# Kernel tuning notes

Hardware: AMD Instinct MI355X
Metric: run time of the kernel (lower is better)

The kernel has to match this reference:

```python
import jax, jax.numpy as jnp
import numpy as np
from jax import lax

B, T, L = 16, 200, 250
IDIM, ODIM, DUNITS = 512, 80, 1024
ATT_DIM, ACONV_CHANS, ACONV_K = 128, 32, 31
PRENET = 256


def setup_inputs() -> dict:
    key = jax.random.key(0)
    ks = iter(jax.random.split(key, 40))
    def nrm(shape, fan_in):
        return jax.random.normal(next(ks), shape, jnp.float32) * (fan_in ** -0.5)
    inp = {}
    inp['hs'] = jax.random.normal(next(ks), (B, T, IDIM), jnp.float32)
    inp['hlens'] = jax.random.randint(next(ks), (B,), T // 2, T + 1)
    inp['ys'] = jax.random.normal(next(ks), (B, L, ODIM), jnp.float32)
    # location-aware attention params
    inp['W_enc'] = nrm((IDIM, ATT_DIM), IDIM)
    inp['b_enc'] = jnp.zeros((ATT_DIM,), jnp.float32)
    inp['W_dec'] = nrm((DUNITS, ATT_DIM), DUNITS)
    inp['W_att'] = nrm((ACONV_CHANS, ATT_DIM), ACONV_CHANS)
    inp['loc_conv_w'] = nrm((ACONV_CHANS, 1, ACONV_K), ACONV_K)
    inp['gvec_w'] = nrm((ATT_DIM,), ATT_DIM)
    inp['gvec_b'] = jnp.zeros((), jnp.float32)
    # prenet (no bias, dropout off in eval)
    inp['prenet_W1'] = nrm((ODIM, PRENET), ODIM)
    inp['prenet_W2'] = nrm((PRENET, PRENET), PRENET)
    # LSTM cells (torch gate order i,f,g,o; bih+bhh folded into one bias)
    in0 = IDIM + PRENET
    inp['Wih0'] = nrm((4 * DUNITS, in0), in0)
    inp['Whh0'] = nrm((4 * DUNITS, DUNITS), DUNITS)
    inp['b0'] = jnp.zeros((4 * DUNITS,), jnp.float32)
    inp['Wih1'] = nrm((4 * DUNITS, DUNITS), DUNITS)
    inp['Whh1'] = nrm((4 * DUNITS, DUNITS), DUNITS)
    inp['b1'] = jnp.zeros((4 * DUNITS,), jnp.float32)
    # output heads
    inp['feat_W'] = nrm((DUNITS, ODIM), DUNITS)
    inp['prob_W'] = nrm((DUNITS,), DUNITS)
    inp['prob_b'] = jnp.zeros((), jnp.float32)
    # postnet: conv(no bias) + BN(eval; running mean=0, var=1 folded away) + tanh
    inp['post_w_in'] = nrm((512, ODIM, 5), 5 * ODIM)
    inp['post_g_in'] = jnp.ones((512,), jnp.float32)
    inp['post_b_in'] = jnp.zeros((512,), jnp.float32)
    inp['post_w_mid'] = nrm((3, 512, 512, 5), 5 * 512)
    inp['post_g_mid'] = jnp.ones((3, 512), jnp.float32)
    inp['post_b_mid'] = jnp.zeros((3, 512), jnp.float32)
    inp['post_w_out'] = nrm((ODIM, 512, 5), 5 * 512)
    inp['post_g_out'] = jnp.ones((ODIM,), jnp.float32)
    inp['post_b_out'] = jnp.zeros((ODIM,), jnp.float32)
    return inp


def _conv1d(x, w, pad):
    # x: [B, Cin, T], w: [Cout, Cin, K]
    return lax.conv_general_dilated(x, w, (1,), [(pad, pad)],
                                    dimension_numbers=('NCH', 'OIH', 'NCH'))


def _lstm(x, h, c, Wih, Whh, b):
    g = x @ Wih.T + h @ Whh.T + b
    i, f, gg, o = jnp.split(g, 4, axis=-1)
    c2 = jax.nn.sigmoid(f) * c + jax.nn.sigmoid(i) * jnp.tanh(gg)
    return jax.nn.sigmoid(o) * jnp.tanh(c2), c2


def reference(hs, hlens, ys, W_enc, b_enc, W_dec, W_att, loc_conv_w, gvec_w, gvec_b,
              prenet_W1, prenet_W2, Wih0, Whh0, b0, Wih1, Whh1, b1,
              feat_W, prob_W, prob_b,
              post_w_in, post_g_in, post_b_in, post_w_mid, post_g_mid, post_b_mid,
              post_w_out, post_g_out, post_b_out):
    mask = jnp.arange(T)[None, :] < hlens[:, None]            # [B,T]
    pre_enc = hs @ W_enc + b_enc                              # [B,T,A] precomputed
    # teacher forcing: prenet input at step i is ys[:, i-1] (zeros at i=0);
    # prenet has no recurrent dependency -> vectorize over time
    prev = jnp.concatenate([jnp.zeros((B, 1, ODIM), hs.dtype), ys[:, :L - 1]], axis=1)
    pren = jax.nn.relu(jax.nn.relu(prev @ prenet_W1) @ prenet_W2)  # [B,L,256]
    att_w0 = mask.astype(hs.dtype) / hlens[:, None].astype(hs.dtype)
    z = jnp.zeros((B, DUNITS), hs.dtype)
    carry0 = (z, z, z, z, att_w0)

    def step(carry, pren_t):
        z0, c0, z1, c1, att_w = carry
        conv = _conv1d(att_w[:, None, :], loc_conv_w, ACONV_K // 2)   # [B,C,T]
        e = jnp.tanh(pre_enc + jnp.einsum('bct,ca->bta', conv, W_att)
                     + (z0 @ W_dec)[:, None, :]) @ gvec_w + gvec_b    # [B,T]
        e = jnp.where(mask, e, -1e30)
        w = jax.nn.softmax(2.0 * e, axis=1)                           # scaling=2.0
        att_c = jnp.einsum('bt,btd->bd', w, hs)
        x = jnp.concatenate([att_c, pren_t], axis=1)
        z0n, c0n = _lstm(x, z0, c0, Wih0, Whh0, b0)
        z1n, c1n = _lstm(z0n, z1, c1, Wih1, Whh1, b1)
        return (z0n, c0n, z1n, c1n, w), (z1n @ feat_W, z1n @ prob_W + prob_b)

    _, (outs, probs) = lax.scan(step, carry0, jnp.swapaxes(pren, 0, 1))
    outs = jnp.transpose(outs, (1, 2, 0))   # [B, odim, L] (matches torch.stack dim=2)
    probs = probs.T                         # [B, L]
    # postnet (BN in eval with running mean=0/var=1 reduces to gamma*x+beta)
    h = jnp.tanh(post_g_in[:, None] * _conv1d(outs, post_w_in, 2) + post_b_in[:, None])
    for i in range(3):
        h = jnp.tanh(post_g_mid[i][:, None] * _conv1d(h, post_w_mid[i], 2)
                     + post_b_mid[i][:, None])
    h = post_g_out[:, None] * _conv1d(h, post_w_out, 2) + post_b_out[:, None]
    post_outs = outs + h
    return jnp.swapaxes(post_outs, 1, 2), jnp.swapaxes(outs, 1, 2), probs
```

## Files before the change

kernel.cpp:

```cpp
#include <hip/hip_runtime.h>
#include <cstdint>
#include <cstddef>

constexpr int B_ = 16, T_ = 200, L_ = 250;
constexpr int IDIM = 512, ODIM = 80, DUNITS = 1024;
constexpr int ADIM = 128, ACH = 32, AK = 31;
constexpr int PRE = 256;
constexpr int TPAD = 208;

typedef _Float16 h16;
typedef _Float16 half8 __attribute__((ext_vector_type(8)));
typedef _Float16 half4 __attribute__((ext_vector_type(4)));
typedef float f32x4 __attribute__((ext_vector_type(4)));

constexpr int FSTEP = 800;
constexpr int FZ0W = 0, FDPW = 256, FAW = 288;

constexpr size_t OFF_PE    = 0;
constexpr size_t OFF_H0H   = 851968;
constexpr size_t OFF_Z1H   = 917504;
constexpr size_t OFF_ATTC  = 983040;
constexpr size_t OFF_DP    = 999424;
constexpr size_t OFF_FLAGS = 1007616;
constexpr size_t ZERO_BYTES= 1807616;
constexpr size_t OFF_MB    = 1807616;
constexpr size_t OFF_WDR   = 1815808;
constexpr size_t OFF_PREN  = 2077952;
constexpr size_t OFF_HSH   = 4125952;
constexpr size_t OFF_W0AH  = 7402752;
constexpr size_t OFF_WHH0  = 13694208;
constexpr size_t OFF_WI1   = 22082816;
constexpr size_t OFF_WHH1  = 30471424;
constexpr size_t OFF_Z1ALL = 38860032;
constexpr size_t OFF_OUTS  = 47052032;
constexpr size_t OFF_PA    = 48332032;
constexpr size_t OFF_PB    = 56524032;

__device__ __forceinline__ float fsig(float x) {
  x = fminf(fmaxf(x, -30.f), 30.f);
  return __builtin_amdgcn_rcpf(1.f + __expf(-x));
}
__device__ __forceinline__ float ftanh(float x) {
  x = fminf(fmaxf(x, -15.f), 15.f);
  const float e = __expf(2.f * x);
  return (e - 1.f) * __builtin_amdgcn_rcpf(e + 1.f);
}
__device__ __forceinline__ f32x4 mfma16(half8 a, half8 b, f32x4 c) {
  return __builtin_amdgcn_mfma_f32_16x16x32_f16(a, b, c, 0, 0, 0);
}
__device__ __forceinline__ half8 load8_agent(const h16* p) {
  union { unsigned long long q[2]; half8 v; } cv;
  cv.q[0] = __hip_atomic_load((const unsigned long long*)p, __ATOMIC_RELAXED,
                              __HIP_MEMORY_SCOPE_AGENT);
  cv.q[1] = __hip_atomic_load(((const unsigned long long*)p) + 1, __ATOMIC_RELAXED,
                              __HIP_MEMORY_SCOPE_AGENT);
  return cv.v;
}
__device__ __forceinline__ float loadf_agent(const float* p) {
  union { unsigned u; float f; } cv;
  cv.u = __hip_atomic_load((const unsigned*)p, __ATOMIC_RELAXED,
                           __HIP_MEMORY_SCOPE_AGENT);
  return cv.f;
}
__device__ __forceinline__ void storef_agent(float* p, float v) {
  union { unsigned u; float f; } cv; cv.f = v;
  __hip_atomic_store((unsigned*)p, cv.u, __ATOMIC_RELAXED, __HIP_MEMORY_SCOPE_AGENT);
}
__device__ __forceinline__ int loadw(const int* p) {
  return __hip_atomic_load(p, __ATOMIC_RELAXED, __HIP_MEMORY_SCOPE_AGENT);
}
__device__ __forceinline__ void storew(int* p, int v) {
  __hip_atomic_store(p, v, __ATOMIC_RELAXED, __HIP_MEMORY_SCOPE_AGENT);
}
__device__ __forceinline__ void poll_n(const int* base, const int n) {
  if ((int)threadIdx.x < n) {
    const int* f = base + threadIdx.x;
    while (loadw(f) == 0) __builtin_amdgcn_s_sleep(1);
  }
  __syncthreads();
  __builtin_amdgcn_sched_barrier(0);
}
__device__ __forceinline__ void poll_all256(const int* base) {
  const int* f = base + threadIdx.x;
  while (loadw(f) == 0) __builtin_amdgcn_s_sleep(1);
  __syncthreads();
  __builtin_amdgcn_sched_barrier(0);
}


__global__ void k_zero(float4* __restrict__ p, int n4) {
  const int i = blockIdx.x * blockDim.x + threadIdx.x;
  if (i < n4) p[i] = make_float4(0.f, 0.f, 0.f, 0.f);
}

__global__ void __launch_bounds__(128) k_preenc(const float* __restrict__ hs,
    const float* __restrict__ W_enc, const float* __restrict__ b_enc,
    h16* __restrict__ pe_h) {
  const int bt = blockIdx.x, b = bt / T_, tt = bt % T_;
  __shared__ float s[IDIM];
  for (int i = threadIdx.x; i < IDIM; i += 128) s[i] = hs[(size_t)bt * IDIM + i];
  __syncthreads();
  const int a = threadIdx.x;
  float acc = b_enc[a];
#pragma unroll 4
  for (int d = 0; d < IDIM; ++d) acc += s[d] * W_enc[d * ADIM + a];
  pe_h[((size_t)b * ADIM + a) * TPAD + tt] = (h16)acc;
}

__global__ void k_precMb(const float* __restrict__ lconv, const float* __restrict__ W_att,
                         h16* __restrict__ Mb) {
  const int at = blockIdx.x, lane = threadIdx.x;
  const int a = at * 16 + (lane & 15);
  const int k0 = (lane >> 4) * 8;
  half8 o;
#pragma unroll
  for (int j = 0; j < 8; ++j) {
    const int k = k0 + j;
    float v = 0.f;
    if (k < AK)
      for (int c = 0; c < ACH; ++c) v += lconv[c * AK + k] * W_att[c * ADIM + a];
    o[j] = (h16)v;
  }
  *(half8*)(Mb + (size_t)(at * 64 + lane) * 8) = o;
}

__global__ void k_cvt_perm(const float* __restrict__ src, h16* __restrict__ dst,
                           const int K) {
  const int rr = blockIdx.x;
  const int u = rr >> 2, g = rr & 3;
  const float* s = src + (size_t)(g * 1024 + u) * K;
  h16* d = dst + (size_t)rr * K;
  for (int k = threadIdx.x; k < K; k += 256) d[k] = (h16)s[k];
}

__global__ void k_cvt_wdec(const float* __restrict__ Wdec, h16* __restrict__ Wdr) {
  const int a = blockIdx.x;
  for (int k = threadIdx.x; k < 1024; k += 256)
    Wdr[(size_t)a * 1024 + k] = (h16)Wdec[(size_t)k * ADIM + a];
}

__global__ void k_cvt_f32f16(const float* __restrict__ src, h16* __restrict__ dst) {
  const size_t i = ((size_t)blockIdx.x * 256 + threadIdx.x) * 4;
  const float4 v = *(const float4*)(src + i);
  half4 o; o[0] = (h16)v.x; o[1] = (h16)v.y; o[2] = (h16)v.z; o[3] = (h16)v.w;
  *(half4*)(dst + i) = o;
}

__global__ void k_prenet1(const float* __restrict__ ys, const float* __restrict__ W1,
                          float* __restrict__ h1) {
  const int bl = blockIdx.x, b = bl / L_, l = bl % L_;
  __shared__ float s[ODIM];
  if (threadIdx.x < ODIM)
    s[threadIdx.x] = (l == 0) ? 0.f : ys[((size_t)b * L_ + l - 1) * ODIM + threadIdx.x];
  __syncthreads();
  const int p = threadIdx.x;
  float acc = 0.f;
#pragma unroll 4
  for (int o = 0; o < ODIM; ++o) acc += s[o] * W1[o * PRE + p];
  h1[(size_t)bl * PRE + p] = fmaxf(acc, 0.f);
}

__global__ void k_prenet2h(const float* __restrict__ h1, const float* __restrict__ W2,
                           h16* __restrict__ pren_h) {
  const int bl = blockIdx.x, b = bl / L_, ll = bl % L_;
  __shared__ float s[PRE];
  s[threadIdx.x] = h1[(size_t)bl * PRE + threadIdx.x];
  __syncthreads();
  const int p = threadIdx.x;
  float acc = 0.f;
#pragma unroll 4
  for (int o = 0; o < PRE; ++o) acc += s[o] * W2[o * PRE + p];
  pren_h[((size_t)ll * B_ + b) * PRE + p] = (h16)fmaxf(acc, 0.f);
}


struct ScanP {
  const h16 *pe_h, *Mb, *Wdr, *hs_h, *pren_h;
  const h16 *W0ah, *Whh0h, *Wz01h, *Whh1h;
  h16 *h0h, *z1h, *attc;
  float *dp;
  const float *gvw, *b0, *b1;
  const int *hlens;
  h16 *z1all;
  int *flags;
};

__device__ __forceinline__ void lstm0_partA(const h16* pren_t, const h16* z0p,
    const half8 wA[6], const half8 wH[8], f32x4& acc) {
  const int lane = threadIdx.x & 63, wave = threadIdx.x >> 6;
  const int nloc = lane & 15, kl8 = (lane >> 4) * 8;
  half8 rz[8];
#pragma unroll
  for (int c = 0; c < 8; ++c)
    rz[c] = load8_agent(z0p + nloc * DUNITS + wave * 256 + c * 32 + kl8);
#pragma unroll
  for (int c = 0; c < 8; ++c) acc = mfma16(rz[c], wH[c], acc);
#pragma unroll
  for (int c = 0; c < 6; ++c) {
    const int kg = wave * 192 + c * 32;
    if (kg >= 512)
      acc = mfma16(*(const half8*)(pren_t + nloc * PRE + (kg - 512) + kl8), wA[c], acc);
  }
}

__device__ __forceinline__ void lstm0_partB(const ScanP& P,
    h16* z0o, const int slab, const half8 wA[6], float& c0reg, f32x4 acc,
    float sred[4][64][5], float sg[16][20], h16* sho) {
  const int tid = threadIdx.x;
  const int lane = tid & 63, wave = tid >> 6;
  const int nloc = lane & 15, kl8 = (lane >> 4) * 8;
  half8 ra[6];
#pragma unroll
  for (int c = 0; c < 6; ++c) {
    const int kg = wave * 192 + c * 32;
    if (kg < 512) ra[c] = load8_agent(P.attc + nloc * IDIM + kg + kl8);
  }
#pragma unroll
  for (int c = 0; c < 6; ++c) {
    const int kg = wave * 192 + c * 32;
    if (kg < 512) acc = mfma16(ra[c], wA[c], acc);
  }
#pragma unroll
  for (int r = 0; r < 4; ++r) sred[wave][lane][r] = acc[r];
  __syncthreads();
  {
    const float v = sred[0][lane][wave] + sred[1][lane][wave]
                  + sred[2][lane][wave] + sred[3][lane][wave];
    sg[lane & 15][4 * (lane >> 4) + wave] = v;
  }
  __syncthreads();
  if (tid < 64) {
    const int ul = tid >> 4, b = tid & 15;
    const int u = slab * 4 + ul;
    const float xi = sg[ul * 4 + 0][b] + P.b0[u];
    const float xf = sg[ul * 4 + 1][b] + P.b0[1024 + u];
    const float xg = sg[ul * 4 + 2][b] + P.b0[2048 + u];
    const float xo = sg[ul * 4 + 3][b] + P.b0[3072 + u];
    const float cn = fsig(xf) * c0reg + fsig(xi) * ftanh(xg);
    c0reg = cn;
    sho[ul * 16 + b] = (h16)(fsig(xo) * ftanh(cn));
  }
  __syncthreads();
  if (tid < 16) {
    union { h16 h[4]; unsigned long long q; } u4;
#pragma unroll
    for (int j = 0; j < 4; ++j) u4.h[j] = sho[j * 16 + tid];
    __hip_atomic_store((unsigned long long*)(z0o + tid * DUNITS + slab * 4), u4.q,
                       __ATOMIC_RELAXED, __HIP_MEMORY_SCOPE_AGENT);
  }
}

__device__ __forceinline__ void lstm1_mm(const ScanP& P, const half8 r0[8],
    const half8 r1[8], h16* z1o, h16* z1all_s, const int slab,
    const half8 wI[8], const half8 wHH[8], float& c1reg,
    float sred[4][64][5], float sg[16][20], h16* sho) {
  const int tid = threadIdx.x;
  const int lane = tid & 63, wave = tid >> 6;
  f32x4 acc = {0.f, 0.f, 0.f, 0.f};
#pragma unroll
  for (int c = 0; c < 8; ++c) acc = mfma16(r0[c], wI[c], acc);
#pragma unroll
  for (int c = 0; c < 8; ++c) acc = mfma16(r1[c], wHH[c], acc);
#pragma unroll
  for (int r = 0; r < 4; ++r) sred[wave][lane][r] = acc[r];
  __syncthreads();
  {
    const float v = sred[0][lane][wave] + sred[1][lane][wave]
                  + sred[2][lane][wave] + sred[3][lane][wave];
    sg[lane & 15][4 * (lane >> 4) + wave] = v;
  }
  __syncthreads();
  if (tid < 64) {
    const int ul = tid >> 4, b = tid & 15;
    const int u = slab * 4 + ul;
    const float xi = sg[ul * 4 + 0][b] + P.b1[u];
    const float xf = sg[ul * 4 + 1][b] + P.b1[1024 + u];
    const float xg = sg[ul * 4 + 2][b] + P.b1[2048 + u];
    const float xo = sg[ul * 4 + 3][b] + P.b1[3072 + u];
    const float cn = fsig(xf) * c1reg + fsig(xi) * ftanh(xg);
    c1reg = cn;
    const float hn = fsig(xo) * ftanh(cn);
    const h16 hh = (h16)hn;
    z1all_s[b * DUNITS + u] = hh;
    sho[ul * 16 + b] = hh;
  }
  __syncthreads();
  if (tid < 16) {
    union { h16 h[4]; unsigned long long q; } u4;
#pragma unroll
    for (int j = 0; j < 4; ++j) u4.h[j] = sho[j * 16 + tid];
    __hip_atomic_store((unsigned long long*)(z1o + tid * DUNITS + slab * 4), u4.q,
                       __ATOMIC_RELAXED, __HIP_MEMORY_SCOPE_AGENT);
  }
}

__global__ void __launch_bounds__(256, 1) k_scan(const ScanP P) {
  __shared__ float s_red[4][64][5];
  __shared__ float s_g[16][20];
  __shared__ h16   s_ho[64];
  __shared__ float s_aw[240];
  __shared__ float s_dp[ADIM];
  __shared__ float s_gv[ADIM];
  __shared__ float s_ew[256];
  __shared__ float s_wt[208];
  __shared__ float s_par[4][512];
  __shared__ float s_r8[8];
  __shared__ float s_bc[2];
  __shared__ float s_cvpe[13][8][64][4];

  const int blk = blockIdx.x, tid = threadIdx.x;
  const int lane = tid & 63, wave = tid >> 6;
  constexpr int BD = B_ * DUNITS;

  if (blk < 16) {
    const int b = blk;
    const int hl = P.hlens[b];
    const int mtmax = (hl + 15) >> 4;
    const int slab = 240 + b;
    const int l15 = lane & 15;
    half8 bfrag[8];
#pragma unroll
    for (int at = 0; at < 8; ++at)
      bfrag[at] = *(const half8*)(P.Mb + (size_t)(at * 64 + lane) * 8);
    half8 wA[6], wH[8];
    {
      const int nloc = lane & 15, kl8 = (lane >> 4) * 8;
      const h16* wrA = P.W0ah + ((size_t)(slab * 16 + nloc)) * 768 + wave * 192 + kl8;
      const h16* wrH = P.Whh0h + ((size_t)(slab * 16 + nloc)) * 1024 + wave * 256 + kl8;
#pragma unroll
      for (int c = 0; c < 6; ++c) wA[c] = *(const half8*)(wrA + c * 32);
#pragma unroll
      for (int c = 0; c < 8; ++c) wH[c] = *(const half8*)(wrH + c * 32);
    }
    if (tid < 240) {
      const int tt = tid - 15;
      s_aw[tid] = (tt >= 0 && tt < hl) ? (1.f / (float)hl) : 0.f;
    }
    if (tid < ADIM) s_gv[tid] = P.gvw[tid];
    __syncthreads();
    float c0reg = 0.f;

    for (int mi = 0; mi < 4; ++mi) {
      const int mt = wave + mi * 4;
      if (mt < mtmax) {
        half8 af;
#pragma unroll
        for (int j = 0; j < 8; ++j)
          af[j] = (h16)s_aw[mt * 16 + l15 + (lane >> 4) * 8 + j];
        const int t0 = mt * 16 + 4 * (lane >> 4);
        half4 pe[8];
#pragma unroll
        for (int at = 0; at < 8; ++at)
          pe[at] = *(const half4*)(P.pe_h + ((size_t)b * ADIM + at * 16 + l15) * TPAD + t0);
#pragma unroll
        for (int at = 0; at < 8; ++at) {
          f32x4 z4 = {0.f, 0.f, 0.f, 0.f};
          const f32x4 cv = mfma16(af, bfrag[at], z4);
          float4 o;
          o.x = cv[0] + (float)pe[at][0]; o.y = cv[1] + (float)pe[at][1];
          o.z = cv[2] + (float)pe[at][2]; o.w = cv[3] + (float)pe[at][3];
          *(float4*)&s_cvpe[mt][at][lane][0] = o;
        }
      }
    }
    __syncthreads();

    for (int i = 0; i < L_; ++i) {
      const h16* z0p = P.h0h + (size_t)(i & 1) * BD;
      h16* z0o = P.h0h + (size_t)((i & 1) ^ 1) * BD;
      int* sf = P.flags + (size_t)i * FSTEP;
      poll_n(sf + FDPW, 8);
      if (tid < ADIM) s_dp[tid] = loadf_agent(P.dp + b * ADIM + tid);
      __syncthreads();
#pragma unroll
      for (int mi = 0; mi < 4; ++mi) {
        const int mt = wave + mi * 4;
        if (mt < mtmax) {
          const int t0 = mt * 16 + 4 * (lane >> 4);
          float e0 = 0.f, e1 = 0.f, e2 = 0.f, e3 = 0.f;
#pragma unroll
          for (int at = 0; at < 8; ++at) {
            const float4 v = *(const float4*)&s_cvpe[mt][at][lane][0];
            const int a = at * 16 + l15;
            const float g = s_gv[a], d = s_dp[a];
            e0 += g * ftanh(v.x + d);
            e1 += g * ftanh(v.y + d);
            e2 += g * ftanh(v.z + d);
            e3 += g * ftanh(v.w + d);
          }
#pragma unroll
          for (int o = 1; o < 16; o <<= 1) {
            e0 += __shfl_xor(e0, o); e1 += __shfl_xor(e1, o);
            e2 += __shfl_xor(e2, o); e3 += __shfl_xor(e3, o);
          }
          if (l15 == 0) {
            s_ew[t0 + 0] = e0; s_ew[t0 + 1] = e1; s_ew[t0 + 2] = e2; s_ew[t0 + 3] = e3;
          }
        }
      }
      __syncthreads();
      const float val = (tid < hl) ? 2.f * s_ew[tid] : -3.0e38f;
      float m = val;
#pragma unroll
      for (int o = 32; o > 0; o >>= 1) m = fmaxf(m, __shfl_xor(m, o));
      if ((tid & 63) == 0) s_r8[tid >> 6] = m;
      __syncthreads();
      if (tid == 0) s_bc[0] = fmaxf(fmaxf(s_r8[0], s_r8[1]), fmaxf(s_r8[2], s_r8[3]));
      __syncthreads();
      const float pp = (tid < hl) ? __expf(val - s_bc[0]) : 0.f;
      float ssum = pp;
#pragma unroll
      for (int o = 32; o > 0; o >>= 1) ssum += __shfl_xor(ssum, o);
      if ((tid & 63) == 0) s_r8[4 + (tid >> 6)] = ssum;
      __syncthreads();
      if (tid == 0) s_bc[1] = __builtin_amdgcn_rcpf(s_r8[4] + s_r8[5] + s_r8[6] + s_r8[7]);
      __syncthreads();
      if (tid < T_) {
        const float w = pp * s_bc[1];
        s_wt[tid] = w;
        s_aw[15 + tid] = w;
      }
      __syncthreads();
      const h16* hsb = P.hs_h + (size_t)b * T_ * IDIM;
      {
        const int d0 = lane * 8;
        const h16* hp = hsb + d0;
        float a8[8] = {0.f, 0.f, 0.f, 0.f, 0.f, 0.f, 0.f, 0.f};
        int tt = wave;
        for (; tt + 12 < hl; tt += 16) {
          const half8 h0 = *(const half8*)(hp + (size_t)tt * IDIM);
          const half8 h1 = *(const half8*)(hp + (size_t)(tt + 4) * IDIM);
          const half8 h2 = *(const half8*)(hp + (size_t)(tt + 8) * IDIM);
          const half8 h3 = *(const half8*)(hp + (size_t)(tt + 12) * IDIM);
          const float w0 = s_wt[tt], w1 = s_wt[tt + 4];
          const float w2 = s_wt[tt + 8], w3 = s_wt[tt + 12];
#pragma unroll
          for (int j = 0; j < 8; ++j)
            a8[j] += w0 * (float)h0[j] + w1 * (float)h1[j]
                   + w2 * (float)h2[j] + w3 * (float)h3[j];
        }
        for (; tt < hl; tt += 4) {
          const half8 hv = *(const half8*)(hp + (size_t)tt * IDIM);
          const float wt = s_wt[tt];
#pragma unroll
          for (int j = 0; j < 8; ++j) a8[j] += wt * (float)hv[j];
        }
#pragma unroll
        for (int j = 0; j < 8; ++j) s_par[wave][d0 + j] = a8[j];
      }
      __syncthreads();
      {
        const int d = tid * 2;
        const float cx0 = s_par[0][d] + s_par[1][d] + s_par[2][d] + s_par[3][d];
        const float cx1 = s_par[0][d + 1] + s_par[1][d + 1] + s_par[2][d + 1]
                        + s_par[3][d + 1];
        union { h16 h[2]; unsigned u; } cv;
        cv.h[0] = (h16)cx0; cv.h[1] = (h16)cx1;
        __hip_atomic_store((unsigned*)(P.attc + b * IDIM + d), cv.u,
                           __ATOMIC_RELAXED, __HIP_MEMORY_SCOPE_AGENT);
      }
      asm volatile("s_waitcnt vmcnt(0)" ::: "memory");
      __syncthreads();
      if (tid < 16) storew(sf + FAW + tid * 32 + b, 1);
      f32x4 acc0 = {0.f, 0.f, 0.f, 0.f};
      lstm0_partA(P.pren_h + (size_t)i * (B_ * PRE), z0p, wA, wH, acc0);
      poll_n(sf + FAW + (blk & 15) * 32, 16);
      lstm0_partB(P, z0o, slab, wA, c0reg, acc0, s_red, s_g, s_ho);
      asm volatile("s_waitcnt vmcnt(0)" ::: "memory");
      __syncthreads();
      if (tid == 0) storew(sf + FZ0W + blk, 1);
      for (int mi = 0; mi < 4; ++mi) {
        const int mt = wave + mi * 4;
        if (mt < mtmax) {
          half8 af;
#pragma unroll
          for (int j = 0; j < 8; ++j)
            af[j] = (h16)s_aw[mt * 16 + l15 + (lane >> 4) * 8 + j];
          const int t0 = mt * 16 + 4 * (lane >> 4);
          half4 pe[8];
#pragma unroll
          for (int at = 0; at < 8; ++at)
            pe[at] = *(const half4*)(P.pe_h + ((size_t)b * ADIM + at * 16 + l15) * TPAD + t0);
#pragma unroll
          for (int at = 0; at < 8; ++at) {
            f32x4 z4 = {0.f, 0.f, 0.f, 0.f};
            const f32x4 cv = mfma16(af, bfrag[at], z4);
            float4 o;
            o.x = cv[0] + (float)pe[at][0]; o.y = cv[1] + (float)pe[at][1];
            o.z = cv[2] + (float)pe[at][2]; o.w = cv[3] + (float)pe[at][3];
            *(float4*)&s_cvpe[mt][at][lane][0] = o;
          }
        }
      }
      __syncthreads();
    }
    return;
  }

  const int g = blk - 16;
  const bool dbl = (g < 16);
  const bool isdp = (g >= 16 && g < 24);
  half8 wA0[6], wH0[8], wI1a[8], wHH1a[8], wI1b[8], wHH1b[8], wD[8];
  {
    const int nloc = lane & 15, kl8 = (lane >> 4) * 8;
    const h16* wrA = P.W0ah + ((size_t)(g * 16 + nloc)) * 768 + wave * 192 + kl8;
    const h16* wrH = P.Whh0h + ((size_t)(g * 16 + nloc)) * 1024 + wave * 256 + kl8;
    const h16* wrI = P.Wz01h + ((size_t)(g * 16 + nloc)) * 1024 + wave * 256 + kl8;
    const h16* wrX = P.Whh1h + ((size_t)(g * 16 + nloc)) * 1024 + wave * 256 + kl8;
#pragma unroll
    for (int c = 0; c < 6; ++c) wA0[c] = *(const half8*)(wrA + c * 32);
#pragma unroll
    for (int c = 0; c < 8; ++c) wH0[c] = *(const half8*)(wrH + c * 32);
#pragma unroll
    for (int c = 0; c < 8; ++c) wI1a[c] = *(const half8*)(wrI + c * 32);
#pragma unroll
    for (int c = 0; c < 8; ++c) wHH1a[c] = *(const half8*)(wrX + c * 32);
    if (dbl) {
      const h16* wrI2 = P.Wz01h + ((size_t)((240 + g) * 16 + nloc)) * 1024 + wave * 256 + kl8;
      const h16* wrX2 = P.Whh1h + ((size_t)((240 + g) * 16 + nloc)) * 1024 + wave * 256 + kl8;
#pragma unroll
      for (int c = 0; c < 8; ++c) wI1b[c] = *(const half8*)(wrI2 + c * 32);
#pragma unroll
      for (int c = 0; c < 8; ++c) wHH1b[c] = *(const half8*)(wrX2 + c * 32);
    }
    if (isdp) {
      const h16* wrD = P.Wdr + ((size_t)((g - 16) * 16 + nloc)) * 1024 + wave * 256 + kl8;
#pragma unroll
      for (int c = 0; c < 8; ++c) wD[c] = *(const half8*)(wrD + c * 32);
    }
  }
  float c0reg = 0.f, c1a = 0.f, c1b = 0.f;
  const int nloc = lane & 15, kl8 = (lane >> 4) * 8;

  for (int i = 0; i < L_; ++i) {
    const h16* z0p = P.h0h + (size_t)(i & 1) * BD;
    h16* z0o = P.h0h + (size_t)((i & 1) ^ 1) * BD;
    const h16* z1p = P.z1h + (size_t)((i & 1) ^ 1) * BD;
    h16* z1o = P.z1h + (size_t)(i & 1) * BD;
    int* sf = P.flags + (size_t)i * FSTEP;
    if (i > 0) poll_all256(P.flags + (size_t)(i - 1) * FSTEP + FZ0W);
    if (isdp) {
      half8 rz[8];
#pragma unroll
      for (int c = 0; c < 8; ++c)
        rz[c] = load8_agent(z0p + nloc * DUNITS + wave * 256 + c * 32 + kl8);
      f32x4 acc = {0.f, 0.f, 0.f, 0.f};
#pragma unroll
      for (int c = 0; c < 8; ++c) acc = mfma16(rz[c], wD[c], acc);
#pragma unroll
      for (int r = 0; r < 4; ++r) s_red[wave][lane][r] = acc[r];
      __syncthreads();
      {
        const float v = s_red[0][lane][wave] + s_red[1][lane][wave]
                      + s_red[2][lane][wave] + s_red[3][lane][wave];
        const int row = lane & 15, batch = 4 * (lane >> 4) + wave;
        storef_agent(P.dp + batch * ADIM + (g - 16) * 16 + row, v);
      }
      asm volatile("s_waitcnt vmcnt(0)" ::: "memory");
      __syncthreads();
      if (tid == 0) storew(sf + FDPW + (g - 16), 1);
    }
    if (i > 0) {
      half8 r0[8], r1[8];
#pragma unroll
      for (int c = 0; c < 8; ++c)
        r0[c] = load8_agent(z0p + nloc * DUNITS + wave * 256 + c * 32 + kl8);
#pragma unroll
      for (int c = 0; c < 8; ++c)
        r1[c] = load8_agent(z1p + nloc * DUNITS + wave * 256 + c * 32 + kl8);
      h16* z1s = P.z1all + (size_t)(i - 1) * BD;
      lstm1_mm(P, r0, r1, z1o, z1s, g, wI1a, wHH1a, c1a, s_red, s_g, s_ho);
      if (dbl)
        lstm1_mm(P, r0, r1, z1o, z1s, 240 + g, wI1b, wHH1b, c1b, s_red, s_g, s_ho);
    }
    f32x4 acc0 = {0.f, 0.f, 0.f, 0.f};
    lstm0_partA(P.pren_h + (size_t)i * (B_ * PRE), z0p, wA0, wH0, acc0);
    poll_n(sf + FAW + (blk & 15) * 32, 16);
    lstm0_partB(P, z0o, g, wA0, c0reg, acc0, s_red, s_g, s_ho);
    asm volatile("s_waitcnt vmcnt(0)" ::: "memory");
    __syncthreads();
    if (tid == 0) storew(sf + FZ0W + blk, 1);
  }
  poll_all256(P.flags + (size_t)(L_ - 1) * FSTEP + FZ0W);
  {
    const h16* z0p = P.h0h + (size_t)(L_ & 1) * BD;
    const h16* z1p = P.z1h + (size_t)((L_ & 1) ^ 1) * BD;
    h16* z1o = P.z1h + (size_t)(L_ & 1) * BD;
    h16* z1s = P.z1all + (size_t)(L_ - 1) * BD;
    half8 r0[8], r1[8];
#pragma unroll
    for (int c = 0; c < 8; ++c)
      r0[c] = load8_agent(z0p + nloc * DUNITS + wave * 256 + c * 32 + kl8);
#pragma unroll
    for (int c = 0; c < 8; ++c)
      r1[c] = load8_agent(z1p + nloc * DUNITS + wave * 256 + c * 32 + kl8);
    lstm1_mm(P, r0, r1, z1o, z1s, g, wI1a, wHH1a, c1a, s_red, s_g, s_ho);
    if (dbl)
      lstm1_mm(P, r0, r1, z1o, z1s, 240 + g, wI1b, wHH1b, c1b, s_red, s_g, s_ho);
  }
}


__global__ void __launch_bounds__(128) k_heads(const h16* __restrict__ z1_all,
    const float* __restrict__ feat_W, const float* __restrict__ prob_W,
    const float* __restrict__ prob_b, float* __restrict__ out1,
    float* __restrict__ probs, float* __restrict__ outs_bct) {
  const int bl = blockIdx.x, b = bl / L_, l = bl % L_;
  __shared__ float s_z[DUNITS];
  const h16* z = z1_all + ((size_t)l * B_ + b) * DUNITS;
  for (int i = threadIdx.x; i < DUNITS; i += 128) s_z[i] = (float)z[i];
  __syncthreads();
  const int co = threadIdx.x;
  if (co < ODIM) {
    float acc = 0.f;
#pragma unroll 4
    for (int d = 0; d < DUNITS; ++d) acc += s_z[d] * feat_W[d * ODIM + co];
    out1[((size_t)b * L_ + l) * ODIM + co] = acc;
    outs_bct[((size_t)b * ODIM + co) * L_ + l] = acc;
  } else if (co == 96) {
    float acc = prob_b[0];
#pragma unroll 4
    for (int d = 0; d < DUNITS; ++d) acc += s_z[d] * prob_W[d];
    probs[(size_t)b * L_ + l] = acc;
  }
}

template <bool TANH, bool FINAL>
__global__ void __launch_bounds__(256) k_conv(const float* __restrict__ x,
    const float* __restrict__ w, const float* __restrict__ gamma,
    const float* __restrict__ beta, float* __restrict__ y,
    const float* __restrict__ res, float* __restrict__ out0,
    const int Cin, const int Cout) {
  const int b = blockIdx.x;
  const int co0 = blockIdx.y * 8;
  const int tid = threadIdx.x;
  const int l = tid & 127;
  const int cg = tid >> 7;
  __shared__ float s_x[8][260];
  __shared__ float s_w[8][8][5];
  float acc[4][2] = {{0.f, 0.f}, {0.f, 0.f}, {0.f, 0.f}, {0.f, 0.f}};
  for (int ci0 = 0; ci0 < Cin; ci0 += 8) {
    __syncthreads();
    for (int i = tid; i < 8 * 260; i += 256) {
      const int ci = i / 260, col = i % 260;
      const int ll = col - 2;
      s_x[ci][col] = (ll >= 0 && ll < L_) ? x[((size_t)b * Cin + ci0 + ci) * L_ + ll] : 0.f;
    }
    for (int i = tid; i < 8 * 8 * 5; i += 256) {
      const int ci = i / 40, rem = i % 40, cl = rem / 5, k = rem % 5;
      s_w[ci][cl][k] = w[((size_t)(co0 + cl) * Cin + ci0 + ci) * 5 + k];
    }
    __syncthreads();
#pragma unroll 2
    for (int ci = 0; ci < 8; ++ci) {
      float xv0[5], xv1[5];
#pragma unroll
      for (int k = 0; k < 5; ++k) { xv0[k] = s_x[ci][l + k]; xv1[k] = s_x[ci][l + 128 + k]; }
#pragma unroll
      for (int j = 0; j < 4; ++j) {
        const int cl = cg * 4 + j;
#pragma unroll
        for (int k = 0; k < 5; ++k) {
          const float ww = s_w[ci][cl][k];
          acc[j][0] += ww * xv0[k];
          acc[j][1] += ww * xv1[k];
        }
      }
    }
  }
#pragma unroll
  for (int j = 0; j < 4; ++j) {
    const int co = co0 + cg * 4 + j;
    const float gm = gamma[co], bt = beta[co];
#pragma unroll
    for (int h = 0; h < 2; ++h) {
      const int ll = l + h * 128;
      if (ll < L_) {
        float v = gm * acc[j][h] + bt;
        if (TANH) v = ftanh(v);
        if (FINAL) out0[((size_t)b * L_ + ll) * ODIM + co] =
                       res[((size_t)b * ODIM + co) * L_ + ll] + v;
        else y[((size_t)b * Cout + co) * L_ + ll] = v;
      }
    }
  }
}


extern "C" void kernel_launch(void* const* d_in, const int* in_sizes, int n_in,
                              void* d_out, int out_size, void* d_ws, size_t ws_size,
                              hipStream_t stream) {
  const float* hs    = (const float*)d_in[0];
  const int*   hlens = (const int*)d_in[1];
  const float* ys    = (const float*)d_in[2];
  const float* W_enc = (const float*)d_in[3];
  const float* b_enc = (const float*)d_in[4];
  const float* W_dec = (const float*)d_in[5];
  const float* W_att = (const float*)d_in[6];
  const float* lconv = (const float*)d_in[7];
  const float* gvw   = (const float*)d_in[8];
  const float* pW1   = (const float*)d_in[10];
  const float* pW2   = (const float*)d_in[11];
  const float* Wih0  = (const float*)d_in[12];
  const float* Whh0  = (const float*)d_in[13];
  const float* b0    = (const float*)d_in[14];
  const float* Wih1  = (const float*)d_in[15];
  const float* Whh1  = (const float*)d_in[16];
  const float* b1    = (const float*)d_in[17];
  const float* featW = (const float*)d_in[18];
  const float* probW = (const float*)d_in[19];
  const float* probB = (const float*)d_in[20];
  const float* pwin  = (const float*)d_in[21];
  const float* pgin  = (const float*)d_in[22];
  const float* pbin  = (const float*)d_in[23];
  const float* pwmid = (const float*)d_in[24];
  const float* pgmid = (const float*)d_in[25];
  const float* pbmid = (const float*)d_in[26];
  const float* pwout = (const float*)d_in[27];
  const float* pgout = (const float*)d_in[28];
  const float* pbout = (const float*)d_in[29];

  char* ws = (char*)d_ws;
  h16*   pe_h   = (h16*)(ws + OFF_PE);
  h16*   h0h    = (h16*)(ws + OFF_H0H);
  h16*   z1h    = (h16*)(ws + OFF_Z1H);
  h16*   attc_h = (h16*)(ws + OFF_ATTC);
  float* dp     = (float*)(ws + OFF_DP);
  int*   flags  = (int*)(ws + OFF_FLAGS);
  h16*   Mb     = (h16*)(ws + OFF_MB);
  h16*   Wdr    = (h16*)(ws + OFF_WDR);
  h16*   pren_h = (h16*)(ws + OFF_PREN);
  h16*   hs_h   = (h16*)(ws + OFF_HSH);
  h16*   W0ah   = (h16*)(ws + OFF_W0AH);
  h16*   Whh0h  = (h16*)(ws + OFF_WHH0);
  h16*   Wz01h  = (h16*)(ws + OFF_WI1);
  h16*   Whh1h  = (h16*)(ws + OFF_WHH1);
  h16*   z1all  = (h16*)(ws + OFF_Z1ALL);
  float* outsb  = (float*)(ws + OFF_OUTS);
  float* pa     = (float*)(ws + OFF_PA);
  float* pb     = (float*)(ws + OFF_PB);

  float* out0 = (float*)d_out;
  float* out1 = out0 + (size_t)B_ * L_ * ODIM;
  float* out2 = out1 + (size_t)B_ * L_ * ODIM;

  hipLaunchKernelGGL(k_zero, dim3((ZERO_BYTES / 16 + 255) / 256), dim3(256), 0, stream,
                     (float4*)ws, (int)(ZERO_BYTES / 16));
  hipLaunchKernelGGL(k_preenc, dim3(B_ * T_), dim3(128), 0, stream, hs, W_enc, b_enc, pe_h);
  hipLaunchKernelGGL(k_precMb, dim3(8), dim3(64), 0, stream, lconv, W_att, Mb);
  hipLaunchKernelGGL(k_cvt_perm, dim3(4096), dim3(256), 0, stream, Wih0, W0ah, 768);
  hipLaunchKernelGGL(k_cvt_perm, dim3(4096), dim3(256), 0, stream, Whh0, Whh0h, 1024);
  hipLaunchKernelGGL(k_cvt_perm, dim3(4096), dim3(256), 0, stream, Wih1, Wz01h, 1024);
  hipLaunchKernelGGL(k_cvt_perm, dim3(4096), dim3(256), 0, stream, Whh1, Whh1h, 1024);
  hipLaunchKernelGGL(k_cvt_wdec, dim3(128), dim3(256), 0, stream, W_dec, Wdr);
  hipLaunchKernelGGL(k_cvt_f32f16, dim3(1600), dim3(256), 0, stream, hs, hs_h);
  hipLaunchKernelGGL(k_prenet1, dim3(B_ * L_), dim3(PRE), 0, stream, ys, pW1, pa);
  hipLaunchKernelGGL(k_prenet2h, dim3(B_ * L_), dim3(PRE), 0, stream, pa, pW2, pren_h);

  ScanP S{pe_h, Mb, Wdr, hs_h, pren_h, W0ah, Whh0h, Wz01h, Whh1h,
          h0h, z1h, attc_h, dp, gvw, b0, b1, hlens, z1all, flags};
  hipLaunchKernelGGL(k_scan, dim3(256), dim3(256), 0, stream, S);

  hipLaunchKernelGGL(k_heads, dim3(B_ * L_), dim3(128), 0, stream,
                     z1all, featW, probW, probB, out1, out2, outsb);

  hipLaunchKernelGGL((k_conv<true, false>), dim3(B_, 64), dim3(256), 0, stream,
                     outsb, pwin, pgin, pbin, pa, nullptr, nullptr, ODIM, 512);
  hipLaunchKernelGGL((k_conv<true, false>), dim3(B_, 64), dim3(256), 0, stream,
                     pa, pwmid, pgmid, pbmid, pb, nullptr, nullptr, 512, 512);
  hipLaunchKernelGGL((k_conv<true, false>), dim3(B_, 64), dim3(256), 0, stream,
                     pb, pwmid + (size_t)512 * 512 * 5, pgmid + 512, pbmid + 512,
                     pa, nullptr, nullptr, 512, 512);
  hipLaunchKernelGGL((k_conv<true, false>), dim3(B_, 64), dim3(256), 0, stream,
                     pa, pwmid + (size_t)2 * 512 * 512 * 5, pgmid + 1024, pbmid + 1024,
                     pb, nullptr, nullptr, 512, 512);
  hipLaunchKernelGGL((k_conv<false, true>), dim3(B_, 10), dim3(256), 0, stream,
                     pb, pwout, pgout, pbout, nullptr, outsb, out0, 512, ODIM);
}
```

Baseline: 6.994 ms.

## Compute decoder attention projection locally in attention blocks instead of via dp blocks

Result: slower. 7.307 ms (+4.5%).

```diff
diff --git a/kernel.cpp b/kernel.cpp
--- a/kernel.cpp
+++ b/kernel.cpp
@@ -13,28 +13,27 @@
 typedef _Float16 half4 __attribute__((ext_vector_type(4)));
 typedef float f32x4 __attribute__((ext_vector_type(4)));
 
-constexpr int FSTEP = 800;
-constexpr int FZ0W = 0, FDPW = 256, FAW = 288;
+constexpr int FSTEP = 768;
+constexpr int FZ0W = 0, FAW = 256;
 
 constexpr size_t OFF_PE    = 0;
 constexpr size_t OFF_H0H   = 851968;
 constexpr size_t OFF_Z1H   = 917504;
 constexpr size_t OFF_ATTC  = 983040;
-constexpr size_t OFF_DP    = 999424;
-constexpr size_t OFF_FLAGS = 1007616;
-constexpr size_t ZERO_BYTES= 1807616;
-constexpr size_t OFF_MB    = 1807616;
-constexpr size_t OFF_WDR   = 1815808;
-constexpr size_t OFF_PREN  = 2077952;
-constexpr size_t OFF_HSH   = 4125952;
-constexpr size_t OFF_W0AH  = 7402752;
-constexpr size_t OFF_WHH0  = 13694208;
-constexpr size_t OFF_WI1   = 22082816;
-constexpr size_t OFF_WHH1  = 30471424;
-constexpr size_t OFF_Z1ALL = 38860032;
-constexpr size_t OFF_OUTS  = 47052032;
-constexpr size_t OFF_PA    = 48332032;
-constexpr size_t OFF_PB    = 56524032;
+constexpr size_t OFF_FLAGS = 999424;
+constexpr size_t ZERO_BYTES= 1767424;
+constexpr size_t OFF_MB    = 1767424;
+constexpr size_t OFF_WDH   = 1775616;
+constexpr size_t OFF_PREN  = 2037760;
+constexpr size_t OFF_HSH   = 4085760;
+constexpr size_t OFF_W0AH  = 7362560;
+constexpr size_t OFF_WHH0  = 13654016;
+constexpr size_t OFF_WI1   = 22042624;
+constexpr size_t OFF_WHH1  = 30431232;
+constexpr size_t OFF_Z1ALL = 38819840;
+constexpr size_t OFF_OUTS  = 47011840;
+constexpr size_t OFF_PA    = 48291840;
+constexpr size_t OFF_PB    = 56483840;
 
 __device__ __forceinline__ float fsig(float x) {
   x = fminf(fmaxf(x, -30.f), 30.f);
@@ -56,16 +55,6 @@
                               __HIP_MEMORY_SCOPE_AGENT);
   return cv.v;
 }
-__device__ __forceinline__ float loadf_agent(const float* p) {
-  union { unsigned u; float f; } cv;
-  cv.u = __hip_atomic_load((const unsigned*)p, __ATOMIC_RELAXED,
-                           __HIP_MEMORY_SCOPE_AGENT);
-  return cv.f;
-}
-__device__ __forceinline__ void storef_agent(float* p, float v) {
-  union { unsigned u; float f; } cv; cv.f = v;
-  __hip_atomic_store((unsigned*)p, cv.u, __ATOMIC_RELAXED, __HIP_MEMORY_SCOPE_AGENT);
-}
 __device__ __forceinline__ int loadw(const int* p) {
   return __hip_atomic_load(p, __ATOMIC_RELAXED, __HIP_MEMORY_SCOPE_AGENT);
 }
@@ -133,12 +122,6 @@
   for (int k = threadIdx.x; k < K; k += 256) d[k] = (h16)s[k];
 }
 
-__global__ void k_cvt_wdec(const float* __restrict__ Wdec, h16* __restrict__ Wdr) {
-  const int a = blockIdx.x;
-  for (int k = threadIdx.x; k < 1024; k += 256)
-    Wdr[(size_t)a * 1024 + k] = (h16)Wdec[(size_t)k * ADIM + a];
-}
-
 __global__ void k_cvt_f32f16(const float* __restrict__ src, h16* __restrict__ dst) {
   const size_t i = ((size_t)blockIdx.x * 256 + threadIdx.x) * 4;
   const float4 v = *(const float4*)(src + i);
@@ -175,10 +158,9 @@
 
 
 struct ScanP {
-  const h16 *pe_h, *Mb, *Wdr, *hs_h, *pren_h;
+  const h16 *pe_h, *Mb, *Wdh, *hs_h, *pren_h;
   const h16 *W0ah, *Whh0h, *Wz01h, *Whh1h;
   h16 *h0h, *z1h, *attc;
-  float *dp;
   const float *gvw, *b0, *b1;
   const int *hlens;
   h16 *z1all;
@@ -304,6 +286,7 @@
   __shared__ float s_ew[256];
   __shared__ float s_wt[208];
   __shared__ float s_par[4][512];
+  __shared__ h16   s_z0h[DUNITS];
   __shared__ float s_r8[8];
   __shared__ float s_bc[2];
   __shared__ float s_cvpe[13][8][64][4];
@@ -369,8 +352,39 @@
       const h16* z0p = P.h0h + (size_t)(i & 1) * BD;
       h16* z0o = P.h0h + (size_t)((i & 1) ^ 1) * BD;
       int* sf = P.flags + (size_t)i * FSTEP;
-      poll_n(sf + FDPW, 8);
-      if (tid < ADIM) s_dp[tid] = loadf_agent(P.dp + b * ADIM + tid);
+      if (i > 0) poll_all256(P.flags + (size_t)(i - 1) * FSTEP + FZ0W);
+      if (tid < 128)
+        *(half8*)(s_z0h + tid * 8) = load8_agent(z0p + b * DUNITS + tid * 8);
+      __syncthreads();
+      {
+        const int kq = tid >> 4, ao = (tid & 15) * 8;
+        const h16* wp = P.Wdh + (size_t)(kq * 64) * ADIM + ao;
+        float a8[8] = {0.f, 0.f, 0.f, 0.f, 0.f, 0.f, 0.f, 0.f};
+#pragma unroll
+        for (int k0 = 0; k0 < 64; k0 += 8) {
+          half8 wv[8];
+#pragma unroll
+          for (int j = 0; j < 8; ++j)
+            wv[j] = *(const half8*)(wp + (size_t)(k0 + j) * ADIM);
+#pragma unroll
+          for (int j = 0; j < 8; ++j) {
+            const float z = (float)s_z0h[kq * 64 + k0 + j];
+#pragma unroll
+            for (int q = 0; q < 8; ++q) a8[q] += z * (float)wv[j][q];
+          }
+        }
+        float* s16 = &s_par[0][0];
+#pragma unroll
+        for (int q = 0; q < 8; ++q) s16[kq * 128 + ao + q] = a8[q];
+      }
+      __syncthreads();
+      if (tid < ADIM) {
+        const float* s16 = &s_par[0][0];
+        float s = 0.f;
+#pragma unroll
+        for (int q = 0; q < 16; ++q) s += s16[q * 128 + tid];
+        s_dp[tid] = s;
+      }
       __syncthreads();
 #pragma unroll
       for (int mi = 0; mi < 4; ++mi) {
@@ -499,8 +513,7 @@
 
   const int g = blk - 16;
   const bool dbl = (g < 16);
-  const bool isdp = (g >= 16 && g < 24);
-  half8 wA0[6], wH0[8], wI1a[8], wHH1a[8], wI1b[8], wHH1b[8], wD[8];
+  half8 wA0[6], wH0[8], wI1a[8], wHH1a[8], wI1b[8], wHH1b[8];
   {
     const int nloc = lane & 15, kl8 = (lane >> 4) * 8;
     const h16* wrA = P.W0ah + ((size_t)(g * 16 + nloc)) * 768 + wave * 192 + kl8;
@@ -522,11 +535,6 @@
       for (int c = 0; c < 8; ++c) wI1b[c] = *(const half8*)(wrI2 + c * 32);
 #pragma unroll
       for (int c = 0; c < 8; ++c) wHH1b[c] = *(const half8*)(wrX2 + c * 32);
-    }
-    if (isdp) {
-      const h16* wrD = P.Wdr + ((size_t)((g - 16) * 16 + nloc)) * 1024 + wave * 256 + kl8;
-#pragma unroll
-      for (int c = 0; c < 8; ++c) wD[c] = *(const half8*)(wrD + c * 32);
     }
   }
   float c0reg = 0.f, c1a = 0.f, c1b = 0.f;
@@ -539,27 +547,6 @@
     h16* z1o = P.z1h + (size_t)(i & 1) * BD;
     int* sf = P.flags + (size_t)i * FSTEP;
     if (i > 0) poll_all256(P.flags + (size_t)(i - 1) * FSTEP + FZ0W);
-    if (isdp) {
-      half8 rz[8];
-#pragma unroll
-      for (int c = 0; c < 8; ++c)
-        rz[c] = load8_agent(z0p + nloc * DUNITS + wave * 256 + c * 32 + kl8);
-      f32x4 acc = {0.f, 0.f, 0.f, 0.f};
-#pragma unroll
-      for (int c = 0; c < 8; ++c) acc = mfma16(rz[c], wD[c], acc);
-#pragma unroll
-      for (int r = 0; r < 4; ++r) s_red[wave][lane][r] = acc[r];
-      __syncthreads();
-      {
-        const float v = s_red[0][lane][wave] + s_red[1][lane][wave]
-                      + s_red[2][lane][wave] + s_red[3][lane][wave];
-        const int row = lane & 15, batch = 4 * (lane >> 4) + wave;
-        storef_agent(P.dp + batch * ADIM + (g - 16) * 16 + row, v);
-      }
-      asm volatile("s_waitcnt vmcnt(0)" ::: "memory");
-      __syncthreads();
-      if (tid == 0) storew(sf + FDPW + (g - 16), 1);
-    }
     if (i > 0) {
       half8 r0[8], r1[8];
 #pragma unroll
@@ -725,10 +712,9 @@
   h16*   h0h    = (h16*)(ws + OFF_H0H);
   h16*   z1h    = (h16*)(ws + OFF_Z1H);
   h16*   attc_h = (h16*)(ws + OFF_ATTC);
-  float* dp     = (float*)(ws + OFF_DP);
   int*   flags  = (int*)(ws + OFF_FLAGS);
   h16*   Mb     = (h16*)(ws + OFF_MB);
-  h16*   Wdr    = (h16*)(ws + OFF_WDR);
+  h16*   Wdh    = (h16*)(ws + OFF_WDH);
   h16*   pren_h = (h16*)(ws + OFF_PREN);
   h16*   hs_h   = (h16*)(ws + OFF_HSH);
   h16*   W0ah   = (h16*)(ws + OFF_W0AH);
@@ -752,13 +738,13 @@
   hipLaunchKernelGGL(k_cvt_perm, dim3(4096), dim3(256), 0, stream, Whh0, Whh0h, 1024);
   hipLaunchKernelGGL(k_cvt_perm, dim3(4096), dim3(256), 0, stream, Wih1, Wz01h, 1024);
   hipLaunchKernelGGL(k_cvt_perm, dim3(4096), dim3(256), 0, stream, Whh1, Whh1h, 1024);
-  hipLaunchKernelGGL(k_cvt_wdec, dim3(128), dim3(256), 0, stream, W_dec, Wdr);
+  hipLaunchKernelGGL(k_cvt_f32f16, dim3(128), dim3(256), 0, stream, W_dec, Wdh);
   hipLaunchKernelGGL(k_cvt_f32f16, dim3(1600), dim3(256), 0, stream, hs, hs_h);
   hipLaunchKernelGGL(k_prenet1, dim3(B_ * L_), dim3(PRE), 0, stream, ys, pW1, pa);
   hipLaunchKernelGGL(k_prenet2h, dim3(B_ * L_), dim3(PRE), 0, stream, pa, pW2, pren_h);
 
-  ScanP S{pe_h, Mb, Wdr, hs_h, pren_h, W0ah, Whh0h, Wz01h, Whh1h,
-          h0h, z1h, attc_h, dp, gvw, b0, b1, hlens, z1all, flags};
+  ScanP S{pe_h, Mb, Wdh, hs_h, pren_h, W0ah, Whh0h, Wz01h, Whh1h,
+          h0h, z1h, attc_h, gvw, b0, b1, hlens, z1all, flags};
   hipLaunchKernelGGL(k_scan, dim3(256), dim3(256), 0, stream, S);
 
   hipLaunchKernelGGL(k_heads, dim3(B_ * L_), dim3(128), 0, stream,
```

## Rewrite postnet convolutions as fp16 MFMA implicit GEMMs with channel-last padded layout

Applied to the files above, without the earlier changes.

Result: faster. 6.101 ms (-12.8%).

```diff
diff --git a/kernel.cpp b/kernel.cpp
--- a/kernel.cpp
+++ b/kernel.cpp
@@ -22,19 +22,23 @@
 constexpr size_t OFF_ATTC  = 983040;
 constexpr size_t OFF_DP    = 999424;
 constexpr size_t OFF_FLAGS = 1007616;
-constexpr size_t ZERO_BYTES= 1807616;
-constexpr size_t OFF_MB    = 1807616;
-constexpr size_t OFF_WDR   = 1815808;
-constexpr size_t OFF_PREN  = 2077952;
-constexpr size_t OFF_HSH   = 4125952;
-constexpr size_t OFF_W0AH  = 7402752;
-constexpr size_t OFF_WHH0  = 13694208;
-constexpr size_t OFF_WI1   = 22082816;
-constexpr size_t OFF_WHH1  = 30471424;
-constexpr size_t OFF_Z1ALL = 38860032;
-constexpr size_t OFF_OUTS  = 47052032;
-constexpr size_t OFF_PA    = 48332032;
-constexpr size_t OFF_PB    = 56524032;
+constexpr size_t OFF_XT1   = 1807616;
+constexpr size_t OFF_XTA   = 2888960;
+constexpr size_t OFF_XTB   = 7214336;
+constexpr size_t ZERO_BYTES= 11539712;
+constexpr size_t OFF_MB    = 11539712;
+constexpr size_t OFF_WDR   = 11547904;
+constexpr size_t OFF_PREN  = 11810048;
+constexpr size_t OFF_HSH   = 13858048;
+constexpr size_t OFF_W0AH  = 17134848;
+constexpr size_t OFF_WHH0  = 23426304;
+constexpr size_t OFF_WI1   = 31814912;
+constexpr size_t OFF_WHH1  = 40203520;
+constexpr size_t OFF_Z1ALL = 48592128;
+constexpr size_t OFF_WTIN  = 56784128;
+constexpr size_t OFF_WTMID = 57439488;
+constexpr size_t OFF_WTOUT = 65303808;
+constexpr size_t OFF_PSC   = 65713408;
 
 __device__ __forceinline__ float fsig(float x) {
   x = fminf(fmaxf(x, -30.f), 30.f);
@@ -171,6 +175,79 @@
 #pragma unroll 4
   for (int o = 0; o < PRE; ++o) acc += s[o] * W2[o * PRE + p];
   pren_h[((size_t)ll * B_ + b) * PRE + p] = (h16)fmaxf(acc, 0.f);
+}
+
+__global__ void k_cvt_wpin(const float* __restrict__ w, h16* __restrict__ o) {
+  const int co = blockIdx.x;
+  for (int i = threadIdx.x; i < 640; i += 256) {
+    const int k = i >> 7, ci = i & 127;
+    o[(size_t)co * 640 + i] = (ci < 80) ? (h16)w[((size_t)co * 80 + ci) * 5 + k] : (h16)0.f;
+  }
+}
+__global__ void k_cvt_wpmid(const float* __restrict__ w, h16* __restrict__ o) {
+  const int idx = blockIdx.x;
+  const float* s = w + (size_t)idx * 512 * 5;
+  h16* d = o + (size_t)idx * 2560;
+  for (int i = threadIdx.x; i < 2560; i += 256) {
+    const int k = i >> 9, ci = i & 511;
+    d[i] = (h16)s[(size_t)ci * 5 + k];
+  }
+}
+__global__ void k_cvt_wpout(const float* __restrict__ w, h16* __restrict__ o) {
+  const int co = blockIdx.x;
+  for (int i = threadIdx.x; i < 2560; i += 256) {
+    const int k = i >> 9, ci = i & 511;
+    o[(size_t)co * 2560 + i] = (h16)w[((size_t)co * 512 + ci) * 5 + k];
+  }
+}
+
+template <int CIP, int NK, bool TANH, bool FINAL>
+__global__ void __launch_bounds__(256) k_cvmf(const h16* __restrict__ xT,
+    const h16* __restrict__ wT, const float* __restrict__ gamma,
+    const float* __restrict__ beta, h16* __restrict__ yT,
+    const float* __restrict__ res, float* __restrict__ out0) {
+  __shared__ float s_red[4][64][5];
+  __shared__ float s_g[16][20];
+  constexpr int KTOT = NK * 128;
+  const int b = blockIdx.x, l0 = blockIdx.y * 16, co0 = blockIdx.z * 16;
+  const int tid = threadIdx.x, lane = tid & 63, wave = tid >> 6;
+  const int nloc = lane & 15, kl8 = (lane >> 4) * 8;
+  const h16* wr = wT + (size_t)(co0 + nloc) * KTOT + wave * (NK * 32) + kl8;
+  half8 w[NK];
+#pragma unroll
+  for (int c = 0; c < NK; ++c) w[c] = *(const half8*)(wr + c * 32);
+  f32x4 acc = {0.f, 0.f, 0.f, 0.f};
+  const h16* xb = xT + (size_t)b * 264 * CIP;
+#pragma unroll
+  for (int c = 0; c < NK; ++c) {
+    const int kg = wave * (NK * 32) + c * 32;
+    const int k = kg / CIP, ci = kg & (CIP - 1);
+    const half8 a = *(const half8*)(xb + (size_t)(l0 + nloc + k) * CIP + ci + kl8);
+    acc = mfma16(a, w[c], acc);
+  }
+#pragma unroll
+  for (int r = 0; r < 4; ++r) s_red[wave][lane][r] = acc[r];
+  __syncthreads();
+  {
+    const float v = s_red[0][lane][wave] + s_red[1][lane][wave]
+                  + s_red[2][lane][wave] + s_red[3][lane][wave];
+    s_g[lane & 15][4 * (lane >> 4) + wave] = v;
+  }
+  __syncthreads();
+  {
+    const int co_l = tid & 15, l_l = tid >> 4;
+    const int co = co0 + co_l, l = l0 + l_l;
+    if (l < L_) {
+      float v = gamma[co] * s_g[co_l][l_l] + beta[co];
+      if (TANH) v = ftanh(v);
+      if (FINAL) {
+        const size_t o = ((size_t)b * L_ + l) * ODIM + co;
+        out0[o] = res[o] + v;
+      } else {
+        yT[((size_t)b * 264 + l + 2) * 512 + co] = (h16)v;
+      }
+    }
+  }
 }
 
 
@@ -604,7 +681,7 @@
 __global__ void __launch_bounds__(128) k_heads(const h16* __restrict__ z1_all,
     const float* __restrict__ feat_W, const float* __restrict__ prob_W,
     const float* __restrict__ prob_b, float* __restrict__ out1,
-    float* __restrict__ probs, float* __restrict__ outs_bct) {
+    float* __restrict__ probs, h16* __restrict__ xT1) {
   const int bl = blockIdx.x, b = bl / L_, l = bl % L_;
   __shared__ float s_z[DUNITS];
   const h16* z = z1_all + ((size_t)l * B_ + b) * DUNITS;
@@ -616,73 +693,12 @@
 #pragma unroll 4
     for (int d = 0; d < DUNITS; ++d) acc += s_z[d] * feat_W[d * ODIM + co];
     out1[((size_t)b * L_ + l) * ODIM + co] = acc;
-    outs_bct[((size_t)b * ODIM + co) * L_ + l] = acc;
+    xT1[((size_t)b * 264 + l + 2) * 128 + co] = (h16)acc;
   } else if (co == 96) {
     float acc = prob_b[0];
 #pragma unroll 4
     for (int d = 0; d < DUNITS; ++d) acc += s_z[d] * prob_W[d];
     probs[(size_t)b * L_ + l] = acc;
-  }
-}
-
-template <bool TANH, bool FINAL>
-__global__ void __launch_bounds__(256) k_conv(const float* __restrict__ x,
-    const float* __restrict__ w, const float* __restrict__ gamma,
-    const float* __restrict__ beta, float* __restrict__ y,
-    const float* __restrict__ res, float* __restrict__ out0,
-    const int Cin, const int Cout) {
-  const int b = blockIdx.x;
-  const int co0 = blockIdx.y * 8;
-  const int tid = threadIdx.x;
-  const int l = tid & 127;
-  const int cg = tid >> 7;
-  __shared__ float s_x[8][260];
-  __shared__ float s_w[8][8][5];
-  float acc[4][2] = {{0.f, 0.f}, {0.f, 0.f}, {0.f, 0.f}, {0.f, 0.f}};
-  for (int ci0 = 0; ci0 < Cin; ci0 += 8) {
-    __syncthreads();
-    for (int i = tid; i < 8 * 260; i += 256) {
-      const int ci = i / 260, col = i % 260;
-      const int ll = col - 2;
-      s_x[ci][col] = (ll >= 0 && ll < L_) ? x[((size_t)b * Cin + ci0 + ci) * L_ + ll] : 0.f;
-    }
-    for (int i = tid; i < 8 * 8 * 5; i += 256) {
-      const int ci = i / 40, rem = i % 40, cl = rem / 5, k = rem % 5;
-      s_w[ci][cl][k] = w[((size_t)(co0 + cl) * Cin + ci0 + ci) * 5 + k];
-    }
-    __syncthreads();
-#pragma unroll 2
-    for (int ci = 0; ci < 8; ++ci) {
-      float xv0[5], xv1[5];
-#pragma unroll
-      for (int k = 0; k < 5; ++k) { xv0[k] = s_x[ci][l + k]; xv1[k] = s_x[ci][l + 128 + k]; }
-#pragma unroll
-      for (int j = 0; j < 4; ++j) {
-        const int cl = cg * 4 + j;
-#pragma unroll
-        for (int k = 0; k < 5; ++k) {
-          const float ww = s_w[ci][cl][k];
-          acc[j][0] += ww * xv0[k];
-          acc[j][1] += ww * xv1[k];
-        }
-      }
-    }
-  }
-#pragma unroll
-  for (int j = 0; j < 4; ++j) {
-    const int co = co0 + cg * 4 + j;
-    const float gm = gamma[co], bt = beta[co];
-#pragma unroll
-    for (int h = 0; h < 2; ++h) {
-      const int ll = l + h * 128;
-      if (ll < L_) {
-        float v = gm * acc[j][h] + bt;
-        if (TANH) v = ftanh(v);
-        if (FINAL) out0[((size_t)b * L_ + ll) * ODIM + co] =
-                       res[((size_t)b * ODIM + co) * L_ + ll] + v;
-        else y[((size_t)b * Cout + co) * L_ + ll] = v;
-      }
-    }
   }
 }
 
@@ -727,6 +743,9 @@
   h16*   attc_h = (h16*)(ws + OFF_ATTC);
   float* dp     = (float*)(ws + OFF_DP);
   int*   flags  = (int*)(ws + OFF_FLAGS);
+  h16*   xT1    = (h16*)(ws + OFF_XT1);
+  h16*   xTA    = (h16*)(ws + OFF_XTA);
+  h16*   xTB    = (h16*)(ws + OFF_XTB);
   h16*   Mb     = (h16*)(ws + OFF_MB);
   h16*   Wdr    = (h16*)(ws + OFF_WDR);
   h16*   pren_h = (h16*)(ws + OFF_PREN);
@@ -736,9 +755,10 @@
   h16*   Wz01h  = (h16*)(ws + OFF_WI1);
   h16*   Whh1h  = (h16*)(ws + OFF_WHH1);
   h16*   z1all  = (h16*)(ws + OFF_Z1ALL);
-  float* outsb  = (float*)(ws + OFF_OUTS);
-  float* pa     = (float*)(ws + OFF_PA);
-  float* pb     = (float*)(ws + OFF_PB);
+  h16*   wTin   = (h16*)(ws + OFF_WTIN);
+  h16*   wTmid  = (h16*)(ws + OFF_WTMID);
+  h16*   wTout  = (h16*)(ws + OFF_WTOUT);
+  float* psc    = (float*)(ws + OFF_PSC);
 
   float* out0 = (float*)d_out;
   float* out1 = out0 + (size_t)B_ * L_ * ODIM;
@@ -754,26 +774,29 @@
   hipLaunchKernelGGL(k_cvt_perm, dim3(4096), dim3(256), 0, stream, Whh1, Whh1h, 1024);
   hipLaunchKernelGGL(k_cvt_wdec, dim3(128), dim3(256), 0, stream, W_dec, Wdr);
   hipLaunchKernelGGL(k_cvt_f32f16, dim3(1600), dim3(256), 0, stream, hs, hs_h);
-  hipLaunchKernelGGL(k_prenet1, dim3(B_ * L_), dim3(PRE), 0, stream, ys, pW1, pa);
-  hipLaunchKernelGGL(k_prenet2h, dim3(B_ * L_), dim3(PRE), 0, stream, pa, pW2, pren_h);
+  hipLaunchKernelGGL(k_prenet1, dim3(B_ * L_), dim3(PRE), 0, stream, ys, pW1, psc);
+  hipLaunchKernelGGL(k_prenet2h, dim3(B_ * L_), dim3(PRE), 0, stream, psc, pW2, pren_h);
+  hipLaunchKernelGGL(k_cvt_wpin, dim3(512), dim3(256), 0, stream, pwin, wTin);
+  hipLaunchKernelGGL(k_cvt_wpmid, dim3(3 * 512), dim3(256), 0, stream, pwmid, wTmid);
+  hipLaunchKernelGGL(k_cvt_wpout, dim3(80), dim3(256), 0, stream, pwout, wTout);
 
   ScanP S{pe_h, Mb, Wdr, hs_h, pren_h, W0ah, Whh0h, Wz01h, Whh1h,
           h0h, z1h, attc_h, dp, gvw, b0, b1, hlens, z1all, flags};
   hipLaunchKernelGGL(k_scan, dim3(256), dim3(256), 0, stream, S);
 
   hipLaunchKernelGGL(k_heads, dim3(B_ * L_), dim3(128), 0, stream,
-                     z1all, featW, probW, probB, out1, out2, outsb);
-
-  hipLaunchKernelGGL((k_conv<true, false>), dim3(B_, 64), dim3(256), 0, stream,
-                     outsb, pwin, pgin, pbin, pa, nullptr, nullptr, ODIM, 512);
-  hipLaunchKernelGGL((k_conv<true, false>), dim3(B_, 64), dim3(256), 0, stream,
-                     pa, pwmid, pgmid, pbmid, pb, nullptr, nullptr, 512, 512);
-  hipLaunchKernelGGL((k_conv<true, false>), dim3(B_, 64), dim3(256), 0, stream,
-                     pb, pwmid + (size_t)512 * 512 * 5, pgmid + 512, pbmid + 512,
-                     pa, nullptr, nullptr, 512, 512);
-  hipLaunchKernelGGL((k_conv<true, false>), dim3(B_, 64), dim3(256), 0, stream,
-                     pa, pwmid + (size_t)2 * 512 * 512 * 5, pgmid + 1024, pbmid + 1024,
-                     pb, nullptr, nullptr, 512, 512);
-  hipLaunchKernelGGL((k_conv<false, true>), dim3(B_, 10), dim3(256), 0, stream,
-                     pb, pwout, pgout, pbout, nullptr, outsb, out0, 512, ODIM);
-}
+                     z1all, featW, probW, probB, out1, out2, xT1);
+
+  hipLaunchKernelGGL((k_cvmf<128, 5, true, false>), dim3(16, 16, 32), dim3(256), 0, stream,
+                     xT1, wTin, pgin, pbin, xTA, nullptr, nullptr);
+  hipLaunchKernelGGL((k_cvmf<512, 20, true, false>), dim3(16, 16, 32), dim3(256), 0, stream,
+                     xTA, wTmid, pgmid, pbmid, xTB, nullptr, nullptr);
+  hipLaunchKernelGGL((k_cvmf<512, 20, true, false>), dim3(16, 16, 32), dim3(256), 0, stream,
+                     xTB, wTmid + (size_t)512 * 2560, pgmid + 512, pbmid + 512,
+                     xTA, nullptr, nullptr);
+  hipLaunchKernelGGL((k_cvmf<512, 20, true, false>), dim3(16, 16, 32), dim3(256), 0, stream,
+                     xTA, wTmid + (size_t)2 * 512 * 2560, pgmid + 1024, pbmid + 1024,
+                     xTB, nullptr, nullptr);
+  hipLaunchKernelGGL((k_cvmf<512, 20, false, true>), dim3(16, 16, 5), dim3(256), 0, stream,
+                     xTB, wTout, pgout, pbout, nullptr, out1, out0);
+}
```
